# Kernel tuning notes

Measured on AMD Instinct MI355X. Metric: run time of the kernel, lower is better.

## Reference

```python
import jax, jax.numpy as jnp
import numpy as np

IMG = 224
NUM_VIEWS = 6
K = 5  # splat kernel size (5x5 = 25 offsets)


def setup_inputs() -> dict:
    key = jax.random.key(0)
    points = jax.random.normal(key, (16, 32768, 3), dtype=jnp.float32)
    return {"points": points}


def _render(points):
    B, N, _ = points.shape
    deg2rad = jnp.pi / 180.0
    az = jnp.linspace(0.0, 360.0, NUM_VIEWS + 1)[:-1] * deg2rad          # (V,)
    el = jnp.array([0.0, 30.0, -30.0, 0.0, 0.0, 0.0])[:NUM_VIEWS] * deg2rad

    # 5x5 splat offsets in normalized coords, matching torch meshgrid(ij) + stack([dx,dy])
    off = jnp.linspace(-2.0 / IMG, 2.0 / IMG, K)
    dyg, dxg = jnp.meshgrid(off, off, indexing="ij")
    koff = jnp.stack([dxg, dyg], axis=-1).reshape(-1, 2)                  # (25, 2)

    def one_view(a, e):
        x, y, z = points[..., 0], points[..., 1], points[..., 2]
        x_rot = x * jnp.cos(a) - z * jnp.sin(a)
        z_rot = x * jnp.sin(a) + z * jnp.cos(a)
        y_rot = y * jnp.cos(e) - z_rot * jnp.sin(e)
        z_fin = y * jnp.sin(e) + z_rot * jnp.cos(e)                       # (B, N)
        p2d = jnp.stack([x_rot, y_rot], axis=-1)                          # (B, N, 2)

        zmin = jnp.min(z_fin, axis=1, keepdims=True)
        zmax = jnp.max(z_fin, axis=1, keepdims=True)
        feat = 0.3 + 0.7 * (z_fin - zmin) / (zmax - zmin + 1e-6)          # (B, N), in [0.3, 1.0]

        coords = p2d[:, :, None, :] + koff[None, None, :, :]              # (B, N, 25, 2)
        # torch .long() truncates toward zero; astype(int32) does too
        px = ((coords[..., 0] + 1.0) * 0.5 * (IMG - 1)).astype(jnp.int32)
        py = ((coords[..., 1] + 1.0) * 0.5 * (IMG - 1)).astype(jnp.int32)
        valid = (px >= 0) & (px < IMG) & (py >= 0) & (py < IMG)
        # invalid splats routed out-of-bounds and dropped by the scatter
        idx = jnp.where(valid, py * IMG + px, IMG * IMG).reshape(B, -1)   # (B, N*25)
        f = jnp.broadcast_to(feat[:, :, None], (B, N, K * K)).reshape(B, -1)

        def splat(i, fv):
            return jnp.zeros(IMG * IMG, dtype=points.dtype).at[i].max(fv, mode="drop")

        img = jax.vmap(splat)(idx, f).reshape(B, IMG, IMG)
        # all 3 channels receive the identical feature values
        return jnp.broadcast_to(img[:, None], (B, 3, IMG, IMG))

    views = jax.vmap(one_view)(az, el)                                    # (V, B, 3, H, W)
    return jnp.transpose(views, (1, 0, 2, 3, 4))                          # (B, V, 3, H, W)


def reference(points) -> jnp.ndarray:
    return _render(points)
```

## Files before the change

### kernel.cpp

```cpp
#include <hip/hip_runtime.h>
#include <math.h>

#define IMG    224
#define NVIEWS 6
#define BATCH  16
#define NPTS   32768
#define PLANE  (IMG * IMG)
#define HROWS  112
#define TILE_ELEMS (HROWS * IMG)
#define NT     1024
#define NWAVES (NT / 64)
#define QCAP   128
#define NWG    (BATCH * NVIEWS * 2)

typedef float fx4 __attribute__((ext_vector_type(4)));

struct ViewTrig {
    float sa[NVIEWS], ca[NVIEWS], se[NVIEWS], ce[NVIEWS];
    float off0, off4;
};

__device__ __forceinline__ float fmul_(float a, float b) {
#pragma clang fp contract(off)
    return a * b;
}
__device__ __forceinline__ float fadd_(float a, float b) {
#pragma clang fp contract(off)
    return a + b;
}
__device__ __forceinline__ float fsub_(float a, float b) {
#pragma clang fp contract(off)
    return a - b;
}
__device__ __forceinline__ int pix_(float c) {
    return (int)fmul_(fmul_(fadd_(c, 1.0f), 0.5f), 223.0f);
}

__device__ __forceinline__ unsigned fmap_(float f) {
    unsigned b = __float_as_uint(f);
    return b ^ ((unsigned)((int)b >> 31) | 0x80000000u);
}
__device__ __forceinline__ float fmap_inv_(unsigned u) {
    unsigned b = (u & 0x80000000u) ? (u ^ 0x80000000u) : ~u;
    return __uint_as_float(b);
}

__device__ __forceinline__ int lane_prefix_(unsigned long long m) {
    return __builtin_amdgcn_mbcnt_hi((unsigned)(m >> 32),
           __builtin_amdgcn_mbcnt_lo((unsigned)m, 0));
}

__global__ __launch_bounds__(NT, 4) void render_kernel(
    const float* __restrict__ pts, float* __restrict__ out, ViewTrig vt)
{
    extern __shared__ __align__(16) unsigned tile[];
    __shared__ uint2 wq[NWAVES][QCAP];
    __shared__ float smin[NWAVES], smax[NWAVES];

    const int bid  = blockIdx.x;
    const int xcd  = bid & 7;
    const int slot = bid >> 3;
    const int hi   = (slot >= 12) ? 1 : 0;
    const int b    = xcd + 8 * hi;
    const int vh   = slot - 12 * hi;
    const int v    = vh >> 1;
    const int h    = vh & 1;
    const int bv   = b * NVIEWS + v;
    const int row0 = h * HROWS;
    const int row1 = row0 + HROWS - 1;

    const float sa = vt.sa[v], ca = vt.ca[v], se = vt.se[v], ce = vt.ce[v];
    const float off0 = vt.off0, off4 = vt.off4;
    const float4* p4 = (const float4*)(pts + (size_t)b * NPTS * 3);

    const int lane = threadIdx.x & 63;
    const int wave = threadIdx.x >> 6;

    {
        int4* t4 = (int4*)tile;
        for (int i = threadIdx.x; i < TILE_ELEMS / 4; i += NT)
            t4[i] = make_int4(0, 0, 0, 0);
    }
    __syncthreads();

    float zmin = INFINITY, zmax = -INFINITY;
    unsigned qcnt = 0;

    auto drain64 = [&]() {
        qcnt -= 64;
        const uint2 e = wq[wave][qcnt + lane];
        const unsigned fz = e.x, pk = e.y;
        const int cx0 = pk & 255;
        const int cx1 = (pk >> 8) & 255;
        const int r0 = max((int)((pk >> 16) & 255), row0) - row0;
        const int r1 = min((int)(pk >> 24), row1) - row0;
        #pragma unroll
        for (int dy = 0; dy < 3; ++dy) {
            const int ry = r0 + dy;
            const bool yok = (ry <= r1);
            #pragma unroll
            for (int dx = 0; dx < 3; ++dx) {
                const int cx = cx0 + dx;
                if (yok && (cx <= cx1)) atomicMax(&tile[ry * IMG + cx], fz);
            }
        }
    };

    auto do_point = [&](float x, float y, float z) {
        const float zr = fadd_(fmul_(x, sa), fmul_(z, ca));
        const float yr = fsub_(fmul_(y, ce), fmul_(zr, se));
        const float xr = fsub_(fmul_(x, ca), fmul_(z, sa));

        const int x0i = pix_(fadd_(xr, off0));
        const int x1i = pix_(fadd_(xr, off4));
        const int y0i = pix_(fadd_(yr, off0));
        const int y1i = pix_(fadd_(yr, off4));

        const float zf = fmaf(zr, ce, y * se);
        zmin = fminf(zmin, zf);
        zmax = fmaxf(zmax, zf);

        const bool pred = (x1i >= 0) && (x0i <= IMG - 1) &&
                          (y1i >= row0) && (y0i <= row1);
        const unsigned long long m = __ballot(pred);
        if (pred) {
            const int cx0 = min(max(x0i, 0), IMG - 1);
            const int cx1 = min(max(x1i, 0), IMG - 1);
            const int cy0 = min(max(y0i, 0), IMG - 1);
            const int cy1 = min(max(y1i, 0), IMG - 1);
            const unsigned pk = (unsigned)cx0 | ((unsigned)cx1 << 8) |
                                ((unsigned)cy0 << 16) | ((unsigned)cy1 << 24);
            wq[wave][qcnt + lane_prefix_(m)] = make_uint2(fmap_(zf), pk);
        }
        qcnt += (unsigned)__popcll(m);
        if (qcnt >= 64) drain64();
    };

    #pragma unroll
    for (int k = 0; k < NPTS / (4 * NT); ++k) {
        const int g = threadIdx.x + k * NT;
        const float4 A = p4[3 * g + 0];
        const float4 B = p4[3 * g + 1];
        const float4 C = p4[3 * g + 2];
        do_point(A.x, A.y, A.z);
        do_point(A.w, B.x, B.y);
        do_point(B.z, B.w, C.x);
        do_point(C.y, C.z, C.w);
    }

    if (lane < (int)qcnt) {
        const uint2 e = wq[wave][lane];
        const unsigned fz = e.x, pk = e.y;
        const int cx0 = pk & 255;
        const int cx1 = (pk >> 8) & 255;
        const int r0 = max((int)((pk >> 16) & 255), row0) - row0;
        const int r1 = min((int)(pk >> 24), row1) - row0;
        #pragma unroll
        for (int dy = 0; dy < 3; ++dy) {
            const int ry = r0 + dy;
            const bool yok = (ry <= r1);
            #pragma unroll
            for (int dx = 0; dx < 3; ++dx) {
                const int cx = cx0 + dx;
                if (yok && (cx <= cx1)) atomicMax(&tile[ry * IMG + cx], fz);
            }
        }
    }

    for (int o = 32; o > 0; o >>= 1) {
        zmin = fminf(zmin, __shfl_down(zmin, o, 64));
        zmax = fmaxf(zmax, __shfl_down(zmax, o, 64));
    }
    if (lane == 0) { smin[wave] = zmin; smax[wave] = zmax; }
    __syncthreads();
    if (threadIdx.x == 0) {
        float mn = smin[0], mx = smax[0];
        for (int w = 1; w < NWAVES; ++w) {
            mn = fminf(mn, smin[w]);
            mx = fmaxf(mx, smax[w]);
        }
        smin[0] = mn; smax[0] = mx;
    }
    __syncthreads();
    const float scale = 0.7f / ((smax[0] - smin[0]) + 1e-6f);
    const float bias  = 0.3f - smin[0] * scale;

    float* dst = out + ((size_t)bv * 3) * PLANE + (size_t)row0 * IMG;
    const uint4* src = (const uint4*)tile;
    for (int i = threadIdx.x; i < TILE_ELEMS / 4; i += NT) {
        const uint4 u = src[i];
        fx4 f;
        f.x = (u.x == 0u) ? 0.0f : fmaf(fmap_inv_(u.x), scale, bias);
        f.y = (u.y == 0u) ? 0.0f : fmaf(fmap_inv_(u.y), scale, bias);
        f.z = (u.z == 0u) ? 0.0f : fmaf(fmap_inv_(u.z), scale, bias);
        f.w = (u.w == 0u) ? 0.0f : fmaf(fmap_inv_(u.w), scale, bias);
        #pragma unroll
        for (int c = 0; c < 3; ++c)
            __builtin_nontemporal_store(f, (fx4*)(dst + (size_t)c * PLANE) + i);
    }
}

extern "C" void kernel_launch(void* const* d_in, const int* in_sizes, int n_in,
                              void* d_out, int out_size, void* d_ws, size_t ws_size,
                              hipStream_t stream)
{
    const float* pts = (const float*)d_in[0];
    float* out = (float*)d_out;

    ViewTrig vt;
    const float d2r = (float)(M_PI / 180.0);
    const float el_deg[NVIEWS] = {0.0f, 30.0f, -30.0f, 0.0f, 0.0f, 0.0f};
    for (int v = 0; v < NVIEWS; ++v) {
        float a = (float)(60 * v) * d2r;
        float e = el_deg[v] * d2r;
        vt.sa[v] = (float)sin((double)a);
        vt.ca[v] = (float)cos((double)a);
        vt.se[v] = (float)sin((double)e);
        vt.ce[v] = (float)cos((double)e);
    }
    {
        const float s = (float)(2.0 / 224.0);
        vt.off0 = -s;
        vt.off4 = s;
    }

    (void)hipFuncSetAttribute(reinterpret_cast<const void*>(render_kernel),
                              hipFuncAttributeMaxDynamicSharedMemorySize,
                              TILE_ELEMS * (int)sizeof(int));

    render_kernel<<<NWG, NT, TILE_ELEMS * sizeof(int), stream>>>(pts, out, vt);
}
```

Baseline: 88.54 us.

## Split render into transform/binning kernel and splat kernel via workspace bins

Splits the fused kernel in two. The first kernel transforms points across more workgroups, bins splat entries per image half into global workspace segments, and records per-segment z min/max. The second kernel reads the bins via a prefix-sum lookup, applies atomicMax into the LDS tile, and normalizes the output. This aims to spread the transform over more parallelism and stop each half-tile workgroup from redundantly transforming all points, at the cost of an extra launch and a round trip of the bins through global memory. pix_ also folds the *0.5*223 into a single multiply by 111.5, which could change rounding at truncation boundaries.

```diff
diff --git a/kernel.cpp b/kernel.cpp
--- a/kernel.cpp
+++ b/kernel.cpp
@@ -8,10 +8,18 @@
 #define PLANE  (IMG * IMG)
 #define HROWS  112
 #define TILE_ELEMS (HROWS * IMG)
-#define NT     1024
-#define NWAVES (NT / 64)
-#define QCAP   128
-#define NWG    (BATCH * NVIEWS * 2)
+
+#define K1_NT    256
+#define K1_CHUNK 8
+#define K1_NWG   (BATCH * NVIEWS * K1_CHUNK)
+#define SEGCAP   1024
+#define NSEG     (K1_CHUNK * 4)
+
+#define K2_NT    1024
+#define K2_NWG   (BATCH * NVIEWS * 2)
+
+#define WS_MM_OFF   24576
+#define WS_BIN_OFF  65536
 
 typedef float fx4 __attribute__((ext_vector_type(4)));
 
@@ -33,7 +41,7 @@
     return a - b;
 }
 __device__ __forceinline__ int pix_(float c) {
-    return (int)fmul_(fmul_(fadd_(c, 1.0f), 0.5f), 223.0f);
+    return (int)fmul_(fadd_(c, 1.0f), 111.5f);
 }
 
 __device__ __forceinline__ unsigned fmap_(float f) {
@@ -50,12 +58,98 @@
            __builtin_amdgcn_mbcnt_lo((unsigned)m, 0));
 }
 
-__global__ __launch_bounds__(NT, 4) void render_kernel(
-    const float* __restrict__ pts, float* __restrict__ out, ViewTrig vt)
+__global__ __launch_bounds__(K1_NT, 3) void transform_kernel(
+    const float* __restrict__ pts, unsigned* __restrict__ ws, ViewTrig vt)
+{
+    const int bid   = blockIdx.x;
+    const int chunk = bid & (K1_CHUNK - 1);
+    const int v     = (bid >> 3) % NVIEWS;
+    const int b     = bid / (K1_CHUNK * NVIEWS);
+    const int bv    = b * NVIEWS + v;
+
+    const float sa = vt.sa[v], ca = vt.ca[v], se = vt.se[v], ce = vt.ce[v];
+    const float off0 = vt.off0, off4 = vt.off4;
+    const float4* p4 = (const float4*)(pts + (size_t)b * NPTS * 3);
+
+    const int tid = threadIdx.x, lane = tid & 63, wave = tid >> 6;
+    const int segi = chunk * 4 + wave;
+
+    unsigned* counts = ws;
+    uint2* minmax = (uint2*)((char*)ws + WS_MM_OFF);
+    uint2* bins   = (uint2*)((char*)ws + WS_BIN_OFF);
+    uint2* seg0 = bins + ((size_t)((bv * 2 + 0) * NSEG + segi)) * SEGCAP;
+    uint2* seg1 = bins + ((size_t)((bv * 2 + 1) * NSEG + segi)) * SEGCAP;
+
+    unsigned q0 = 0, q1 = 0;
+    float zmin = INFINITY, zmax = -INFINITY;
+
+    auto do_point = [&](float x, float y, float z) {
+        const float zr = fadd_(fmul_(x, sa), fmul_(z, ca));
+        const float yr = fsub_(fmul_(y, ce), fmul_(zr, se));
+        const float xr = fsub_(fmul_(x, ca), fmul_(z, sa));
+
+        const int x0i = pix_(fadd_(xr, off0));
+        const int x1i = pix_(fadd_(xr, off4));
+        const int y0i = pix_(fadd_(yr, off0));
+        const int y1i = pix_(fadd_(yr, off4));
+
+        const float zf = fmaf(zr, ce, y * se);
+        zmin = fminf(zmin, zf);
+        zmax = fmaxf(zmax, zf);
+
+        const bool okx = (x1i >= 0) && (x0i <= IMG - 1);
+        const bool ok0 = okx && (y1i >= 0)     && (y0i <= HROWS - 1);
+        const bool ok1 = okx && (y1i >= HROWS) && (y0i <= IMG - 1);
+
+        const int cx0 = max(x0i, 0);
+        const int cx1 = min(x1i, IMG - 1);
+        const int cy0 = max(y0i, 0);
+        const int cy1 = min(y1i, IMG - 1);
+        const unsigned pk = (unsigned)cx0 | ((unsigned)cx1 << 8) |
+                            ((unsigned)cy0 << 16) | ((unsigned)cy1 << 24);
+        const unsigned fz = fmap_(zf);
+
+        {
+            const unsigned long long m = __ballot(ok0);
+            if (ok0) seg0[q0 + lane_prefix_(m)] = make_uint2(fz, pk);
+            q0 += (unsigned)__popcll(m);
+        }
+        {
+            const unsigned long long m = __ballot(ok1);
+            if (ok1) seg1[q1 + lane_prefix_(m)] = make_uint2(fz, pk);
+            q1 += (unsigned)__popcll(m);
+        }
+    };
+
+    #pragma unroll
+    for (int kk = 0; kk < 4; ++kk) {
+        const int g = chunk * 1024 + kk * K1_NT + tid;
+        const float4 A = p4[3 * g + 0];
+        const float4 B = p4[3 * g + 1];
+        const float4 C = p4[3 * g + 2];
+        do_point(A.x, A.y, A.z);
+        do_point(A.w, B.x, B.y);
+        do_point(B.z, B.w, C.x);
+        do_point(C.y, C.z, C.w);
+    }
+
+    for (int o = 32; o > 0; o >>= 1) {
+        zmin = fminf(zmin, __shfl_down(zmin, o, 64));
+        zmax = fmaxf(zmax, __shfl_down(zmax, o, 64));
+    }
+    if (lane == 0) {
+        counts[(bv * 2 + 0) * NSEG + segi] = q0;
+        counts[(bv * 2 + 1) * NSEG + segi] = q1;
+        minmax[bv * NSEG + segi] = make_uint2(fmap_(zmax), fmap_(-zmin));
+    }
+}
+
+__global__ __launch_bounds__(K2_NT, 1) void splat_kernel(
+    const unsigned* __restrict__ ws, float* __restrict__ out)
 {
     extern __shared__ __align__(16) unsigned tile[];
-    __shared__ uint2 wq[NWAVES][QCAP];
-    __shared__ float smin[NWAVES], smax[NWAVES];
+    __shared__ unsigned pref[NSEG + 1];
+    __shared__ float sScale, sBias;
 
     const int bid  = blockIdx.x;
     const int xcd  = bid & 7;
@@ -66,30 +160,56 @@
     const int v    = vh >> 1;
     const int h    = vh & 1;
     const int bv   = b * NVIEWS + v;
+    const int bvh  = bv * 2 + h;
     const int row0 = h * HROWS;
     const int row1 = row0 + HROWS - 1;
 
-    const float sa = vt.sa[v], ca = vt.ca[v], se = vt.se[v], ce = vt.ce[v];
-    const float off0 = vt.off0, off4 = vt.off4;
-    const float4* p4 = (const float4*)(pts + (size_t)b * NPTS * 3);
-
-    const int lane = threadIdx.x & 63;
-    const int wave = threadIdx.x >> 6;
+    const int tid = threadIdx.x, lane = tid & 63, wave = tid >> 6;
+
+    const unsigned* counts = ws;
+    const uint2* minmax = (const uint2*)((const char*)ws + WS_MM_OFF);
+    const uint2* binb   = (const uint2*)((const char*)ws + WS_BIN_OFF)
+                        + (size_t)bvh * NSEG * SEGCAP;
 
     {
         int4* t4 = (int4*)tile;
-        for (int i = threadIdx.x; i < TILE_ELEMS / 4; i += NT)
+        for (int i = tid; i < TILE_ELEMS / 4; i += K2_NT)
             t4[i] = make_int4(0, 0, 0, 0);
     }
+    if (wave == 0) {
+        unsigned c = (lane < NSEG) ? counts[bvh * NSEG + lane] : 0u;
+        unsigned inc = c;
+        #pragma unroll
+        for (int o = 1; o < NSEG; o <<= 1) {
+            unsigned t = __shfl_up(inc, o, 64);
+            if (lane >= o) inc += t;
+        }
+        if (lane < NSEG) pref[lane + 1] = inc;
+        if (lane == 0)   pref[0] = 0;
+
+        uint2 mm = (lane < NSEG) ? minmax[bv * NSEG + lane] : make_uint2(0u, 0u);
+        for (int o = 32; o > 0; o >>= 1) {
+            mm.x = max(mm.x, __shfl_down(mm.x, o, 64));
+            mm.y = max(mm.y, __shfl_down(mm.y, o, 64));
+        }
+        if (lane == 0) {
+            const float mx = fmap_inv_(mm.x);
+            const float mn = -fmap_inv_(mm.y);
+            const float scale = 0.7f / ((mx - mn) + 1e-6f);
+            sScale = scale;
+            sBias  = 0.3f - mn * scale;
+        }
+    }
     __syncthreads();
 
-    float zmin = INFINITY, zmax = -INFINITY;
-    unsigned qcnt = 0;
-
-    auto drain64 = [&]() {
-        qcnt -= 64;
-        const uint2 e = wq[wave][qcnt + lane];
-        const unsigned fz = e.x, pk = e.y;
+    const unsigned n = pref[NSEG];
+    for (unsigned e = tid; e < n; e += K2_NT) {
+        int s = 0;
+        #pragma unroll
+        for (int st = 16; st >= 1; st >>= 1)
+            if (pref[s + st] <= e) s += st;
+        const uint2 ent = binb[(size_t)s * SEGCAP + (e - pref[s])];
+        const unsigned fz = ent.x, pk = ent.y;
         const int cx0 = pk & 255;
         const int cx1 = (pk >> 8) & 255;
         const int r0 = max((int)((pk >> 16) & 255), row0) - row0;
@@ -104,90 +224,14 @@
                 if (yok && (cx <= cx1)) atomicMax(&tile[ry * IMG + cx], fz);
             }
         }
-    };
-
-    auto do_point = [&](float x, float y, float z) {
-        const float zr = fadd_(fmul_(x, sa), fmul_(z, ca));
-        const float yr = fsub_(fmul_(y, ce), fmul_(zr, se));
-        const float xr = fsub_(fmul_(x, ca), fmul_(z, sa));
-
-        const int x0i = pix_(fadd_(xr, off0));
-        const int x1i = pix_(fadd_(xr, off4));
-        const int y0i = pix_(fadd_(yr, off0));
-        const int y1i = pix_(fadd_(yr, off4));
-
-        const float zf = fmaf(zr, ce, y * se);
-        zmin = fminf(zmin, zf);
-        zmax = fmaxf(zmax, zf);
-
-        const bool pred = (x1i >= 0) && (x0i <= IMG - 1) &&
-                          (y1i >= row0) && (y0i <= row1);
-        const unsigned long long m = __ballot(pred);
-        if (pred) {
-            const int cx0 = min(max(x0i, 0), IMG - 1);
-            const int cx1 = min(max(x1i, 0), IMG - 1);
-            const int cy0 = min(max(y0i, 0), IMG - 1);
-            const int cy1 = min(max(y1i, 0), IMG - 1);
-            const unsigned pk = (unsigned)cx0 | ((unsigned)cx1 << 8) |
-                                ((unsigned)cy0 << 16) | ((unsigned)cy1 << 24);
-            wq[wave][qcnt + lane_prefix_(m)] = make_uint2(fmap_(zf), pk);
-        }
-        qcnt += (unsigned)__popcll(m);
-        if (qcnt >= 64) drain64();
-    };
-
-    #pragma unroll
-    for (int k = 0; k < NPTS / (4 * NT); ++k) {
-        const int g = threadIdx.x + k * NT;
-        const float4 A = p4[3 * g + 0];
-        const float4 B = p4[3 * g + 1];
-        const float4 C = p4[3 * g + 2];
-        do_point(A.x, A.y, A.z);
-        do_point(A.w, B.x, B.y);
-        do_point(B.z, B.w, C.x);
-        do_point(C.y, C.z, C.w);
-    }
-
-    if (lane < (int)qcnt) {
-        const uint2 e = wq[wave][lane];
-        const unsigned fz = e.x, pk = e.y;
-        const int cx0 = pk & 255;
-        const int cx1 = (pk >> 8) & 255;
-        const int r0 = max((int)((pk >> 16) & 255), row0) - row0;
-        const int r1 = min((int)(pk >> 24), row1) - row0;
-        #pragma unroll
-        for (int dy = 0; dy < 3; ++dy) {
-            const int ry = r0 + dy;
-            const bool yok = (ry <= r1);
-            #pragma unroll
-            for (int dx = 0; dx < 3; ++dx) {
-                const int cx = cx0 + dx;
-                if (yok && (cx <= cx1)) atomicMax(&tile[ry * IMG + cx], fz);
-            }
-        }
-    }
-
-    for (int o = 32; o > 0; o >>= 1) {
-        zmin = fminf(zmin, __shfl_down(zmin, o, 64));
-        zmax = fmaxf(zmax, __shfl_down(zmax, o, 64));
-    }
-    if (lane == 0) { smin[wave] = zmin; smax[wave] = zmax; }
+    }
     __syncthreads();
-    if (threadIdx.x == 0) {
-        float mn = smin[0], mx = smax[0];
-        for (int w = 1; w < NWAVES; ++w) {
-            mn = fminf(mn, smin[w]);
-            mx = fmaxf(mx, smax[w]);
-        }
-        smin[0] = mn; smax[0] = mx;
-    }
-    __syncthreads();
-    const float scale = 0.7f / ((smax[0] - smin[0]) + 1e-6f);
-    const float bias  = 0.3f - smin[0] * scale;
+
+    const float scale = sScale, bias = sBias;
 
     float* dst = out + ((size_t)bv * 3) * PLANE + (size_t)row0 * IMG;
     const uint4* src = (const uint4*)tile;
-    for (int i = threadIdx.x; i < TILE_ELEMS / 4; i += NT) {
+    for (int i = tid; i < TILE_ELEMS / 4; i += K2_NT) {
         const uint4 u = src[i];
         fx4 f;
         f.x = (u.x == 0u) ? 0.0f : fmaf(fmap_inv_(u.x), scale, bias);
@@ -206,6 +250,7 @@
 {
     const float* pts = (const float*)d_in[0];
     float* out = (float*)d_out;
+    unsigned* ws = (unsigned*)d_ws;
 
     ViewTrig vt;
     const float d2r = (float)(M_PI / 180.0);
@@ -224,9 +269,10 @@
         vt.off4 = s;
     }
 
-    (void)hipFuncSetAttribute(reinterpret_cast<const void*>(render_kernel),
+    (void)hipFuncSetAttribute(reinterpret_cast<const void*>(splat_kernel),
                               hipFuncAttributeMaxDynamicSharedMemorySize,
                               TILE_ELEMS * (int)sizeof(int));
 
-    render_kernel<<<NWG, NT, TILE_ELEMS * sizeof(int), stream>>>(pts, out, vt);
-}
+    transform_kernel<<<K1_NWG, K1_NT, 0, stream>>>(pts, ws, vt);
+    splat_kernel<<<K2_NWG, K2_NT, TILE_ELEMS * sizeof(int), stream>>>(ws, out);
+}
```

Measured after the change: 93.78 us. 5.9% more time.
